# Performance work log

Hardware: AMD Instinct MI355X
Metric: run time of the kernel (lower is better)

## Reference

```python
import jax, jax.numpy as jnp
import numpy as np

N_LEVELS = 16
N_FEAT = 2
LOG2_T = 19
TABLE_SIZE = 1 << LOG2_T
COARSE = 16.0
FINE = 512.0
BOX_MIN = jnp.array([-1.0, -1.0, -1.0], jnp.float32)
BOX_MAX = jnp.array([1.0, 1.0, 1.0], jnp.float32)
# corner offsets, bit order (x, y, z) matching utils.BOX_OFFSETS / the trilinear code
OFFSETS = jnp.array([[0, 0, 0], [0, 0, 1], [0, 1, 0], [0, 1, 1],
                     [1, 0, 0], [1, 0, 1], [1, 1, 0], [1, 1, 1]], jnp.int32)
PRIMES = jnp.array([1, 2654435761, 805459861], dtype=jnp.uint32)
_b = np.exp((np.log(FINE) - np.log(COARSE)) / (N_LEVELS - 1))
RESOLUTIONS = jnp.asarray(np.floor(COARSE * _b ** np.arange(N_LEVELS)).astype(np.float32))


def setup_inputs() -> dict:
    key = jax.random.key(0)
    k1, k2 = jax.random.split(key)
    x = jax.random.uniform(k1, (1_000_000, 3), jnp.float32)  # inside the [-1,1]^3 box
    embeddings = jax.random.uniform(k2, (N_LEVELS, TABLE_SIZE, N_FEAT), jnp.float32,
                                    minval=-1e-4, maxval=1e-4)
    return {"x": x, "embeddings": embeddings}


def _hash(corners):
    # corners: (N, 8, 3) int32 -> (N, 8) int32 indices in [0, TABLE_SIZE)
    u = corners.astype(jnp.uint32) * PRIMES  # wraps mod 2^32, matching int32 wrap semantics
    h = u[..., 0] ^ u[..., 1] ^ u[..., 2]
    return (h & jnp.uint32(TABLE_SIZE - 1)).astype(jnp.int32)


def _level(x, table, res):
    grid = (BOX_MAX - BOX_MIN) / res                      # (3,)
    bl = jnp.floor((x - BOX_MIN) / grid).astype(jnp.int32)  # bottom-left voxel index (N,3)
    vmin = bl.astype(jnp.float32) * grid + BOX_MIN
    w = (x - vmin) / grid                                  # trilinear weights (N,3)
    idx = _hash(bl[:, None, :] + OFFSETS[None])            # (N,8)
    emb = table[idx]                                       # (N,8,F) gather
    # per-corner weight = prod over dims of (w if bit else 1-w) — same math as nested lerps
    cw = jnp.prod(jnp.where(OFFSETS[None].astype(bool), w[:, None, :], 1.0 - w[:, None, :]), axis=-1)
    return jnp.einsum('nk,nkf->nf', cw, emb)               # (N,F)


def reference(x, embeddings):
    x = jnp.clip(x, BOX_MIN, BOX_MAX)

    def body(_, lv):
        table, res = lv
        return None, _level(x, table, res)

    _, ys = jax.lax.scan(body, None, (embeddings, RESOLUTIONS))  # (L,N,F)
    return jnp.transpose(ys, (1, 0, 2)).reshape(x.shape[0], N_LEVELS * N_FEAT)
```

## Files before the change

kernel.cpp:

```cpp
#include <hip/hip_runtime.h>
#include <hip/hip_fp16.h>
#include <math.h>

#define N_LEVELS 16
#define LOG2_T 19
#define TABLE_SIZE (1 << LOG2_T)
#define IDX_MASK ((unsigned)(TABLE_SIZE - 1))
#define N_STAGED 4
#define N_FINE (N_LEVELS - N_STAGED)
#define DENSE_CAP 11936
#define THREADS 256
#define PTS_PER_THREAD 4
#define PTS_PER_BLOCK (THREADS * PTS_PER_THREAD)

typedef float f2_t __attribute__((ext_vector_type(2)));
typedef float f4_t __attribute__((ext_vector_type(4)));

struct Params {
    float res[N_LEVELS];
    int   c0[N_STAGED];
    int   K[N_STAGED];
    int   K2[N_STAGED];
    int   base[N_STAGED + 1];
    int   n_pts;
};

__global__ __launch_bounds__(256) void convert_fine(
    const f2_t* __restrict__ emb, unsigned* __restrict__ tab, int n)
{
    int i = blockIdx.x * 256 + threadIdx.x;
    if (i >= n) return;
    f2_t e = __builtin_nontemporal_load(&emb[(size_t)N_STAGED * TABLE_SIZE + i]);
    union { __half2 h2; unsigned u; } c;
    c.h2 = __floats2half2_rn(e.x, e.y);
    __builtin_nontemporal_store(c.u, &tab[i]);
}

__global__ __launch_bounds__(256) void build_dense(
    const f2_t* __restrict__ emb, unsigned* __restrict__ dense, Params P)
{
    int t = blockIdx.x * 256 + threadIdx.x;
    if (t >= P.base[N_STAGED]) return;
    int lev = 0;
    if (t >= P.base[1]) lev = 1;
    if (t >= P.base[2]) lev = 2;
    if (t >= P.base[3]) lev = 3;
    int li = t - P.base[lev];
    int K  = P.K[lev];
    int kx = li % K; int r2 = li / K; int ky = r2 % K; int kz = r2 / K;
    unsigned cx = (unsigned)(P.c0[lev] + kx);
    unsigned cy = (unsigned)(P.c0[lev] + ky);
    unsigned cz = (unsigned)(P.c0[lev] + kz);
    unsigned h = (cx ^ (cy * 2654435761u) ^ (cz * 805459861u)) & IDX_MASK;
    f2_t e = emb[(size_t)lev * TABLE_SIZE + h];
    union { __half2 h2; unsigned u; } c;
    c.h2 = __floats2half2_rn(e.x, e.y);
    dense[t] = c.u;
}

__device__ __forceinline__ void acc_corner(
    unsigned w0, unsigned w1, float g0, float g1, float& a0, float& a1)
{
    union { unsigned u; __half2 h; } p0, p1;
    p0.u = w0; p1.u = w1;
    a0 += g0 * __low2float(p0.h)  + g1 * __low2float(p1.h);
    a1 += g0 * __high2float(p0.h) + g1 * __high2float(p1.h);
}

__device__ __forceinline__ void level_eval(
    int lev, const Params& P, const unsigned* s_dense,
    const unsigned* __restrict__ tabF, const f2_t* __restrict__ emb,
    float xx, float xy, float xz, float& acc0, float& acc1)
{
    float r = P.res[lev];
    float grid = 2.0f / r;
    float tx = (xx + 1.0f) / grid;
    float ty = (xy + 1.0f) / grid;
    float tz = (xz + 1.0f) / grid;
    int blx = (int)floorf(tx);
    int bly = (int)floorf(ty);
    int blz = (int)floorf(tz);
    float wx = (xx - ((float)blx * grid + -1.0f)) / grid;
    float wy = (xy - ((float)bly * grid + -1.0f)) / grid;
    float wz = (xz - ((float)blz * grid + -1.0f)) / grid;

    float fy[2] = {1.0f - wy, wy};
    float fz[2] = {1.0f - wz, wz};
    float fx0 = 1.0f - wx, fx1 = wx;

    acc0 = 0.0f; acc1 = 0.0f;

    if (lev < N_STAGED) {
        int K = P.K[lev], K2 = P.K2[lev], c0 = P.c0[lev];
        int kx = blx - c0, ky = bly - c0, kz = blz - c0;
        unsigned lim = (unsigned)(K - 1);
        if ((unsigned)kx < lim && (unsigned)ky < lim && (unsigned)kz < lim) {
            int i00 = P.base[lev] + (kz * K + ky) * K + kx;
#pragma unroll
            for (int yz = 0; yz < 4; ++yz) {
                int id = i00 + (yz >> 1) * K + (yz & 1) * K2;
                float wyz = fy[yz >> 1] * fz[yz & 1];
                acc_corner(s_dense[id], s_dense[id + 1], fx0 * wyz, fx1 * wyz,
                           acc0, acc1);
            }
        } else {
            const f2_t* tab = emb + (size_t)lev * TABLE_SIZE;
#pragma unroll
            for (int k = 0; k < 8; ++k) {
                int bx = (k >> 2) & 1, by = (k >> 1) & 1, bz = k & 1;
                unsigned cx = (unsigned)(blx + bx);
                unsigned cy = (unsigned)(bly + by);
                unsigned cz = (unsigned)(blz + bz);
                unsigned h = (cx ^ (cy * 2654435761u) ^ (cz * 805459861u)) & IDX_MASK;
                f2_t e = tab[h];
                float w = (bx ? wx : 1.0f - wx) * fy[by] * fz[bz];
                acc0 += w * e.x;
                acc1 += w * e.y;
            }
        }
    } else {
        const unsigned* tab = tabF + (size_t)(lev - N_STAGED) * TABLE_SIZE;
        unsigned ux  = (unsigned)blx;
        unsigned hy0 = (unsigned)bly * 2654435761u;
        unsigned hy1 = ((unsigned)bly + 1u) * 2654435761u;
        unsigned hz0 = (unsigned)blz * 805459861u;
        unsigned hz1 = ((unsigned)blz + 1u) * 805459861u;
        unsigned w0a[4], w1a[4], i1a[4];
#pragma unroll
        for (int yz = 0; yz < 4; ++yz) {
            unsigned hyz = ((yz & 2) ? hy1 : hy0) ^ ((yz & 1) ? hz1 : hz0);
            unsigned i0 = (ux ^ hyz) & IDX_MASK;
            unsigned i1 = ((ux + 1u) ^ hyz) & IDX_MASK;
            i1a[yz] = i1;
            uint4 g = *(const uint4*)(tab + (i0 & ~3u));
            unsigned s0 = i0 & 3u, s1 = i1 & 3u;
            unsigned t0 = (s0 & 1u) ? g.y : g.x;
            unsigned t1 = (s0 & 1u) ? g.w : g.z;
            w0a[yz] = (s0 & 2u) ? t1 : t0;
            unsigned u0 = (s1 & 1u) ? g.y : g.x;
            unsigned u1 = (s1 & 1u) ? g.w : g.z;
            w1a[yz] = (s1 & 2u) ? u1 : u0;
        }
        if ((ux & 3u) == 3u) {
#pragma unroll
            for (int yz = 0; yz < 4; ++yz) w1a[yz] = tab[i1a[yz]];
        }
#pragma unroll
        for (int yz = 0; yz < 4; ++yz) {
            float wyz = fy[yz >> 1] * fz[yz & 1];
            acc_corner(w0a[yz], w1a[yz], fx0 * wyz, fx1 * wyz, acc0, acc1);
        }
    }
}

__global__ __launch_bounds__(256) void ingp_hash_fused(
    const float* __restrict__ x,
    const unsigned* __restrict__ tabF,
    const unsigned* __restrict__ denseG,
    const f2_t* __restrict__ emb,
    float* __restrict__ out,
    Params P)
{
    __shared__ __align__(16) unsigned s_dense[DENSE_CAP];
    {
        const uint4* src = (const uint4*)denseG;
        uint4* dst = (uint4*)s_dense;
#pragma unroll
        for (int i = 0; i < DENSE_CAP / 4 / THREADS + 1; ++i) {
            int id = i * THREADS + (int)threadIdx.x;
            if (id < DENSE_CAP / 4) dst[id] = src[id];
        }
    }
    __syncthreads();

    int base_pt = blockIdx.x * PTS_PER_BLOCK;
#pragma unroll 1
    for (int j = 0; j < PTS_PER_THREAD; ++j) {
        int n = base_pt + j * THREADS + (int)threadIdx.x;
        if (n >= P.n_pts) break;

        float xx = fminf(fmaxf(__builtin_nontemporal_load(&x[n * 3 + 0]), -1.0f), 1.0f);
        float xy = fminf(fmaxf(__builtin_nontemporal_load(&x[n * 3 + 1]), -1.0f), 1.0f);
        float xz = fminf(fmaxf(__builtin_nontemporal_load(&x[n * 3 + 2]), -1.0f), 1.0f);

        float* orow = out + (size_t)n * (N_LEVELS * 2);
#pragma unroll
        for (int lp = 0; lp < N_LEVELS / 2; ++lp) {
            float a0, a1, b0, b1;
            level_eval(2 * lp + 0, P, s_dense, tabF, emb, xx, xy, xz, a0, a1);
            level_eval(2 * lp + 1, P, s_dense, tabF, emb, xx, xy, xz, b0, b1);
            f4_t o4 = {a0, a1, b0, b1};
            __builtin_nontemporal_store(o4, (f4_t*)(orow + lp * 4));
        }
    }
}

__global__ __launch_bounds__(256) void ingp_hash_pair_f32(
    const float* __restrict__ x, const f2_t* __restrict__ emb,
    float* __restrict__ out, Params P)
{
    int b = blockIdx.x;
    int slot = b & 7;
    int n = (b >> 3) * 256 + (int)threadIdx.x;
    if (n >= P.n_pts) return;
    float xx = fminf(fmaxf(x[n * 3 + 0], -1.0f), 1.0f);
    float xy = fminf(fmaxf(x[n * 3 + 1], -1.0f), 1.0f);
    float xz = fminf(fmaxf(x[n * 3 + 2], -1.0f), 1.0f);
    f4_t o4;
#pragma unroll
    for (int hl = 0; hl < 2; ++hl) {
        int lev = 2 * slot + hl;
        float grid = 2.0f / P.res[lev];
        int blx = (int)floorf((xx + 1.0f) / grid);
        int bly = (int)floorf((xy + 1.0f) / grid);
        int blz = (int)floorf((xz + 1.0f) / grid);
        float wx = (xx - ((float)blx * grid + -1.0f)) / grid;
        float wy = (xy - ((float)bly * grid + -1.0f)) / grid;
        float wz = (xz - ((float)blz * grid + -1.0f)) / grid;
        const f2_t* tab = emb + (size_t)lev * TABLE_SIZE;
        float acc0 = 0.0f, acc1 = 0.0f;
#pragma unroll
        for (int k = 0; k < 8; ++k) {
            int bx = (k >> 2) & 1, by = (k >> 1) & 1, bz = k & 1;
            unsigned h = ((unsigned)(blx + bx)
                          ^ ((unsigned)(bly + by) * 2654435761u)
                          ^ ((unsigned)(blz + bz) * 805459861u)) & IDX_MASK;
            f2_t e = tab[h];
            float w = (bx ? wx : 1.0f - wx) * (by ? wy : 1.0f - wy) * (bz ? wz : 1.0f - wz);
            acc0 += w * e.x; acc1 += w * e.y;
        }
        if (hl == 0) { o4.x = acc0; o4.y = acc1; } else { o4.z = acc0; o4.w = acc1; }
    }
    __builtin_nontemporal_store(o4, (f4_t*)(out + (size_t)n * (N_LEVELS * 2) + slot * 4));
}

extern "C" void kernel_launch(void* const* d_in, const int* in_sizes, int n_in,
                              void* d_out, int out_size, void* d_ws, size_t ws_size,
                              hipStream_t stream) {
    const float* x   = (const float*)d_in[0];
    const float* emb = (const float*)d_in[1];
    float* out = (float*)d_out;
    int n_pts = in_sizes[0] / 3;

    Params P;
    double b = exp((log(512.0) - log(16.0)) / 15.0);
    for (int i = 0; i < N_LEVELS; ++i)
        P.res[i] = (float)floor(16.0 * pow(b, (double)i));
    P.n_pts = n_pts;

    int base = 0;
    for (int l = 0; l < N_STAGED; ++l) {
        float grid = 2.0f / P.res[l];
        int blmin = (int)floorf(1.0f / grid);
        int blmax = (int)floorf(2.0f / grid);
        int K = blmax - blmin + 2;
        P.c0[l] = blmin; P.K[l] = K; P.K2[l] = K * K;
        P.base[l] = base; base += K * K * K;
    }
    P.base[N_STAGED] = base;

    size_t need = (size_t)N_FINE * TABLE_SIZE * 4 + (size_t)DENSE_CAP * 4;
    if (base <= DENSE_CAP && ws_size >= need && d_ws != nullptr) {
        unsigned* tabF   = (unsigned*)d_ws;
        unsigned* denseG = tabF + (size_t)N_FINE * TABLE_SIZE;
        int nF = N_FINE * TABLE_SIZE;
        hipLaunchKernelGGL(convert_fine, dim3((nF + 255) / 256), dim3(256), 0, stream,
                           (const f2_t*)emb, tabF, nF);
        hipLaunchKernelGGL(build_dense, dim3((base + 255) / 256), dim3(256), 0, stream,
                           (const f2_t*)emb, denseG, P);
        int blocks = (n_pts + PTS_PER_BLOCK - 1) / PTS_PER_BLOCK;
        hipLaunchKernelGGL(ingp_hash_fused, dim3(blocks), dim3(256), 0, stream,
                           x, tabF, denseG, (const f2_t*)emb, out, P);
    } else {
        int blocks = 8 * ((n_pts + 255) / 256);
        hipLaunchKernelGGL(ingp_hash_pair_f32, dim3(blocks), dim3(256), 0, stream,
                           x, (const f2_t*)emb, out, P);
    }
}
```

Baseline: 628.2 us.

## Split level pairs across threads and stage only two coarse levels in LDS

Each thread now evaluates one pair of levels for a point, with 8 threads per point and 32 points per block iteration. Only levels 0-1 stay in shared memory; levels 2-3 read a 4-aligned dense table from global memory through vector loads. The aim is more parallelism per point, coalesced row writes and a much smaller LDS footprint for higher occupancy. The cost is lane divergence between coarse and fine branches and repeated x loads across the 8 threads of each point.

```diff
diff --git a/kernel.cpp b/kernel.cpp
--- a/kernel.cpp
+++ b/kernel.cpp
@@ -9,9 +9,10 @@
 #define N_STAGED 4
 #define N_FINE (N_LEVELS - N_STAGED)
 #define DENSE_CAP 11936
+#define N_LDS 2728
 #define THREADS 256
-#define PTS_PER_THREAD 4
-#define PTS_PER_BLOCK (THREADS * PTS_PER_THREAD)
+#define ITERS 16
+#define PTS_PER_BLOCK (32 * ITERS)
 
 typedef float f2_t __attribute__((ext_vector_type(2)));
 typedef float f4_t __attribute__((ext_vector_type(4)));
@@ -41,12 +42,13 @@
 {
     int t = blockIdx.x * 256 + threadIdx.x;
     if (t >= P.base[N_STAGED]) return;
-    int lev = 0;
-    if (t >= P.base[1]) lev = 1;
-    if (t >= P.base[2]) lev = 2;
-    if (t >= P.base[3]) lev = 3;
+    int lev = 3;
+    if (t < P.base[3]) lev = 2;
+    if (t < P.base[2]) lev = 1;
+    if (t < P.base[1]) lev = 0;
     int li = t - P.base[lev];
     int K  = P.K[lev];
+    if (li >= K * K * K) return;
     int kx = li % K; int r2 = li / K; int ky = r2 % K; int kz = r2 / K;
     unsigned cx = (unsigned)(P.c0[lev] + kx);
     unsigned cy = (unsigned)(P.c0[lev] + ky);
@@ -67,93 +69,114 @@
     a1 += g0 * __high2float(p0.h) + g1 * __high2float(p1.h);
 }
 
-__device__ __forceinline__ void level_eval(
-    int lev, const Params& P, const unsigned* s_dense,
-    const unsigned* __restrict__ tabF, const f2_t* __restrict__ emb,
-    float xx, float xy, float xz, float& acc0, float& acc1)
-{
-    float r = P.res[lev];
-    float grid = 2.0f / r;
-    float tx = (xx + 1.0f) / grid;
-    float ty = (xy + 1.0f) / grid;
-    float tz = (xz + 1.0f) / grid;
-    int blx = (int)floorf(tx);
-    int bly = (int)floorf(ty);
-    int blz = (int)floorf(tz);
-    float wx = (xx - ((float)blx * grid + -1.0f)) / grid;
-    float wy = (xy - ((float)bly * grid + -1.0f)) / grid;
-    float wz = (xz - ((float)blz * grid + -1.0f)) / grid;
-
-    float fy[2] = {1.0f - wy, wy};
-    float fz[2] = {1.0f - wz, wz};
+__device__ __forceinline__ unsigned pick4(uint4 g, unsigned s)
+{
+    unsigned t0 = (s & 1u) ? g.y : g.x;
+    unsigned t1 = (s & 1u) ? g.w : g.z;
+    return (s & 2u) ? t1 : t0;
+}
+
+#define GRID_SETUP(gridv)                                                  \
+    float tx = (xx + 1.0f) / (gridv);                                      \
+    float ty = (xy + 1.0f) / (gridv);                                      \
+    float tz = (xz + 1.0f) / (gridv);                                      \
+    int blx = (int)floorf(tx);                                             \
+    int bly = (int)floorf(ty);                                             \
+    int blz = (int)floorf(tz);                                             \
+    float wx = (xx - ((float)blx * (gridv) + -1.0f)) / (gridv);            \
+    float wy = (xy - ((float)bly * (gridv) + -1.0f)) / (gridv);            \
+    float wz = (xz - ((float)blz * (gridv) + -1.0f)) / (gridv);            \
+    float fy[2] = {1.0f - wy, wy};                                         \
+    float fz[2] = {1.0f - wz, wz};                                         \
     float fx0 = 1.0f - wx, fx1 = wx;
 
-    acc0 = 0.0f; acc1 = 0.0f;
-
-    if (lev < N_STAGED) {
-        int K = P.K[lev], K2 = P.K2[lev], c0 = P.c0[lev];
-        int kx = blx - c0, ky = bly - c0, kz = blz - c0;
-        unsigned lim = (unsigned)(K - 1);
-        if ((unsigned)kx < lim && (unsigned)ky < lim && (unsigned)kz < lim) {
-            int i00 = P.base[lev] + (kz * K + ky) * K + kx;
+__device__ __forceinline__ void eval_fine(
+    float grid, const unsigned* __restrict__ tab,
+    float xx, float xy, float xz, float& a0, float& a1)
+{
+    GRID_SETUP(grid)
+    unsigned ux  = (unsigned)blx;
+    unsigned hy0 = (unsigned)bly * 2654435761u;
+    unsigned hy1 = ((unsigned)bly + 1u) * 2654435761u;
+    unsigned hz0 = (unsigned)blz * 805459861u;
+    unsigned hz1 = ((unsigned)blz + 1u) * 805459861u;
+    unsigned w0a[4], w1a[4], i1a[4];
+#pragma unroll
+    for (int yz = 0; yz < 4; ++yz) {
+        unsigned hyz = ((yz & 2) ? hy1 : hy0) ^ ((yz & 1) ? hz1 : hz0);
+        unsigned i0 = (ux ^ hyz) & IDX_MASK;
+        unsigned i1 = ((ux + 1u) ^ hyz) & IDX_MASK;
+        i1a[yz] = i1;
+        uint4 g = *(const uint4*)(tab + (i0 & ~3u));
+        w0a[yz] = pick4(g, i0 & 3u);
+        w1a[yz] = pick4(g, i1 & 3u);
+    }
+    if ((ux & 3u) == 3u) {
+#pragma unroll
+        for (int yz = 0; yz < 4; ++yz) w1a[yz] = tab[i1a[yz]];
+    }
+    a0 = 0.0f; a1 = 0.0f;
+#pragma unroll
+    for (int yz = 0; yz < 4; ++yz) {
+        float wyz = fy[yz >> 1] * fz[yz & 1];
+        acc_corner(w0a[yz], w1a[yz], fx0 * wyz, fx1 * wyz, a0, a1);
+    }
+}
+
+template <int LEV, bool FROM_LDS>
+__device__ __forceinline__ void eval_coarse(
+    const Params& P, const unsigned* s_dense, const unsigned* __restrict__ denseG,
+    const f2_t* __restrict__ emb,
+    float xx, float xy, float xz, float& a0, float& a1)
+{
+    float grid = 2.0f / P.res[LEV];
+    GRID_SETUP(grid)
+    int K = P.K[LEV], K2 = P.K2[LEV];
+    int kx = blx - P.c0[LEV], ky = bly - P.c0[LEV], kz = blz - P.c0[LEV];
+    a0 = 0.0f; a1 = 0.0f;
+    unsigned lim = (unsigned)(K - 1);
+    if ((unsigned)kx < lim && (unsigned)ky < lim && (unsigned)kz < lim) {
+        int i00 = (kz * K + ky) * K + kx;
+        if (FROM_LDS) {
+            int ib = P.base[LEV] + i00;
 #pragma unroll
             for (int yz = 0; yz < 4; ++yz) {
-                int id = i00 + (yz >> 1) * K + (yz & 1) * K2;
+                int id = ib + (yz >> 1) * K + (yz & 1) * K2;
                 float wyz = fy[yz >> 1] * fz[yz & 1];
                 acc_corner(s_dense[id], s_dense[id + 1], fx0 * wyz, fx1 * wyz,
-                           acc0, acc1);
+                           a0, a1);
             }
         } else {
-            const f2_t* tab = emb + (size_t)lev * TABLE_SIZE;
-#pragma unroll
-            for (int k = 0; k < 8; ++k) {
-                int bx = (k >> 2) & 1, by = (k >> 1) & 1, bz = k & 1;
-                unsigned cx = (unsigned)(blx + bx);
-                unsigned cy = (unsigned)(bly + by);
-                unsigned cz = (unsigned)(blz + bz);
-                unsigned h = (cx ^ (cy * 2654435761u) ^ (cz * 805459861u)) & IDX_MASK;
-                f2_t e = tab[h];
-                float w = (bx ? wx : 1.0f - wx) * fy[by] * fz[bz];
-                acc0 += w * e.x;
-                acc1 += w * e.y;
+            const unsigned* tb = denseG + P.base[LEV];
+#pragma unroll
+            for (int yz = 0; yz < 4; ++yz) {
+                unsigned id = (unsigned)(i00 + (yz >> 1) * K + (yz & 1) * K2);
+                uint4 g = *(const uint4*)(tb + (id & ~3u));
+                unsigned s0 = id & 3u;
+                unsigned w0 = pick4(g, s0);
+                unsigned w1;
+                if (s0 == 3u) w1 = tb[id + 1u];
+                else          w1 = pick4(g, s0 + 1u);
+                float wyz = fy[yz >> 1] * fz[yz & 1];
+                acc_corner(w0, w1, fx0 * wyz, fx1 * wyz, a0, a1);
             }
         }
     } else {
-        const unsigned* tab = tabF + (size_t)(lev - N_STAGED) * TABLE_SIZE;
-        unsigned ux  = (unsigned)blx;
-        unsigned hy0 = (unsigned)bly * 2654435761u;
-        unsigned hy1 = ((unsigned)bly + 1u) * 2654435761u;
-        unsigned hz0 = (unsigned)blz * 805459861u;
-        unsigned hz1 = ((unsigned)blz + 1u) * 805459861u;
-        unsigned w0a[4], w1a[4], i1a[4];
-#pragma unroll
-        for (int yz = 0; yz < 4; ++yz) {
-            unsigned hyz = ((yz & 2) ? hy1 : hy0) ^ ((yz & 1) ? hz1 : hz0);
-            unsigned i0 = (ux ^ hyz) & IDX_MASK;
-            unsigned i1 = ((ux + 1u) ^ hyz) & IDX_MASK;
-            i1a[yz] = i1;
-            uint4 g = *(const uint4*)(tab + (i0 & ~3u));
-            unsigned s0 = i0 & 3u, s1 = i1 & 3u;
-            unsigned t0 = (s0 & 1u) ? g.y : g.x;
-            unsigned t1 = (s0 & 1u) ? g.w : g.z;
-            w0a[yz] = (s0 & 2u) ? t1 : t0;
-            unsigned u0 = (s1 & 1u) ? g.y : g.x;
-            unsigned u1 = (s1 & 1u) ? g.w : g.z;
-            w1a[yz] = (s1 & 2u) ? u1 : u0;
-        }
-        if ((ux & 3u) == 3u) {
-#pragma unroll
-            for (int yz = 0; yz < 4; ++yz) w1a[yz] = tab[i1a[yz]];
-        }
-#pragma unroll
-        for (int yz = 0; yz < 4; ++yz) {
-            float wyz = fy[yz >> 1] * fz[yz & 1];
-            acc_corner(w0a[yz], w1a[yz], fx0 * wyz, fx1 * wyz, acc0, acc1);
-        }
-    }
-}
-
-__global__ __launch_bounds__(256) void ingp_hash_fused(
+        const f2_t* tab = emb + (size_t)LEV * TABLE_SIZE;
+#pragma unroll
+        for (int k = 0; k < 8; ++k) {
+            int bx = (k >> 2) & 1, by = (k >> 1) & 1, bz = k & 1;
+            unsigned h = ((unsigned)(blx + bx)
+                          ^ ((unsigned)(bly + by) * 2654435761u)
+                          ^ ((unsigned)(blz + bz) * 805459861u)) & IDX_MASK;
+            f2_t e = tab[h];
+            float w = (bx ? wx : 1.0f - wx) * fy[by] * fz[bz];
+            a0 += w * e.x; a1 += w * e.y;
+        }
+    }
+}
+
+__global__ __launch_bounds__(256) void ingp_hash_v5(
     const float* __restrict__ x,
     const unsigned* __restrict__ tabF,
     const unsigned* __restrict__ denseG,
@@ -161,36 +184,51 @@
     float* __restrict__ out,
     Params P)
 {
-    __shared__ __align__(16) unsigned s_dense[DENSE_CAP];
+    __shared__ __align__(16) unsigned s_dense[N_LDS];
+    __shared__ float s_res[N_LEVELS];
     {
         const uint4* src = (const uint4*)denseG;
         uint4* dst = (uint4*)s_dense;
-#pragma unroll
-        for (int i = 0; i < DENSE_CAP / 4 / THREADS + 1; ++i) {
-            int id = i * THREADS + (int)threadIdx.x;
-            if (id < DENSE_CAP / 4) dst[id] = src[id];
-        }
+        for (int id = threadIdx.x; id < N_LDS / 4; id += THREADS) dst[id] = src[id];
+        if (threadIdx.x < N_LEVELS) s_res[threadIdx.x] = P.res[threadIdx.x];
     }
     __syncthreads();
 
-    int base_pt = blockIdx.x * PTS_PER_BLOCK;
+    int lp  = threadIdx.x & 7;
+    int ptl = threadIdx.x >> 3;
+
+    float gridA = 2.0f / s_res[2 * lp];
+    float gridB = 2.0f / s_res[2 * lp + 1];
+    int fo = 2 * lp - 4; if (fo < 0) fo = 0;
+    const unsigned* tA = tabF + (size_t)fo * TABLE_SIZE;
+    const unsigned* tB = tabF + (size_t)(fo + 1) * TABLE_SIZE;
+
+    int base_n = blockIdx.x * PTS_PER_BLOCK + ptl;
+
 #pragma unroll 1
-    for (int j = 0; j < PTS_PER_THREAD; ++j) {
-        int n = base_pt + j * THREADS + (int)threadIdx.x;
-        if (n >= P.n_pts) break;
-
-        float xx = fminf(fmaxf(__builtin_nontemporal_load(&x[n * 3 + 0]), -1.0f), 1.0f);
-        float xy = fminf(fmaxf(__builtin_nontemporal_load(&x[n * 3 + 1]), -1.0f), 1.0f);
-        float xz = fminf(fmaxf(__builtin_nontemporal_load(&x[n * 3 + 2]), -1.0f), 1.0f);
-
-        float* orow = out + (size_t)n * (N_LEVELS * 2);
-#pragma unroll
-        for (int lp = 0; lp < N_LEVELS / 2; ++lp) {
-            float a0, a1, b0, b1;
-            level_eval(2 * lp + 0, P, s_dense, tabF, emb, xx, xy, xz, a0, a1);
-            level_eval(2 * lp + 1, P, s_dense, tabF, emb, xx, xy, xz, b0, b1);
-            f4_t o4 = {a0, a1, b0, b1};
-            __builtin_nontemporal_store(o4, (f4_t*)(orow + lp * 4));
+    for (int it = 0; it < ITERS; ++it) {
+        int n = base_n + it * 32;
+        int nc = n < P.n_pts ? n : P.n_pts - 1;
+        float xx = fminf(fmaxf(__builtin_nontemporal_load(&x[nc * 3 + 0]), -1.0f), 1.0f);
+        float xy = fminf(fmaxf(__builtin_nontemporal_load(&x[nc * 3 + 1]), -1.0f), 1.0f);
+        float xz = fminf(fmaxf(__builtin_nontemporal_load(&x[nc * 3 + 2]), -1.0f), 1.0f);
+
+        float r0, r1, r2, r3;
+        if (lp == 0) {
+            eval_coarse<0, true>(P, s_dense, denseG, emb, xx, xy, xz, r0, r1);
+            eval_coarse<1, true>(P, s_dense, denseG, emb, xx, xy, xz, r2, r3);
+        } else if (lp == 1) {
+            eval_coarse<2, false>(P, s_dense, denseG, emb, xx, xy, xz, r0, r1);
+            eval_coarse<3, false>(P, s_dense, denseG, emb, xx, xy, xz, r2, r3);
+        } else {
+            eval_fine(gridA, tA, xx, xy, xz, r0, r1);
+            eval_fine(gridB, tB, xx, xy, xz, r2, r3);
+        }
+
+        if (n < P.n_pts) {
+            f4_t o4 = {r0, r1, r2, r3};
+            __builtin_nontemporal_store(
+                o4, (f4_t*)(out + (size_t)n * (N_LEVELS * 2) + lp * 4));
         }
     }
 }
@@ -206,7 +244,7 @@
     float xx = fminf(fmaxf(x[n * 3 + 0], -1.0f), 1.0f);
     float xy = fminf(fmaxf(x[n * 3 + 1], -1.0f), 1.0f);
     float xz = fminf(fmaxf(x[n * 3 + 2], -1.0f), 1.0f);
-    f4_t o4;
+    float r0 = 0.f, r1 = 0.f, r2 = 0.f, r3 = 0.f;
 #pragma unroll
     for (int hl = 0; hl < 2; ++hl) {
         int lev = 2 * slot + hl;
@@ -229,8 +267,9 @@
             float w = (bx ? wx : 1.0f - wx) * (by ? wy : 1.0f - wy) * (bz ? wz : 1.0f - wz);
             acc0 += w * e.x; acc1 += w * e.y;
         }
-        if (hl == 0) { o4.x = acc0; o4.y = acc1; } else { o4.z = acc0; o4.w = acc1; }
-    }
+        if (hl == 0) { r0 = acc0; r1 = acc1; } else { r2 = acc0; r3 = acc1; }
+    }
+    f4_t o4 = {r0, r1, r2, r3};
     __builtin_nontemporal_store(o4, (f4_t*)(out + (size_t)n * (N_LEVELS * 2) + slot * 4));
 }
 
@@ -255,12 +294,16 @@
         int blmax = (int)floorf(2.0f / grid);
         int K = blmax - blmin + 2;
         P.c0[l] = blmin; P.K[l] = K; P.K2[l] = K * K;
-        P.base[l] = base; base += K * K * K;
+        P.base[l] = base;
+        base += K * K * K;
+        base = (base + 3) & ~3;
     }
     P.base[N_STAGED] = base;
 
     size_t need = (size_t)N_FINE * TABLE_SIZE * 4 + (size_t)DENSE_CAP * 4;
-    if (base <= DENSE_CAP && ws_size >= need && d_ws != nullptr) {
+    bool ok = (base <= DENSE_CAP) && (P.base[2] == N_LDS) &&
+              (ws_size >= need) && (d_ws != nullptr);
+    if (ok) {
         unsigned* tabF   = (unsigned*)d_ws;
         unsigned* denseG = tabF + (size_t)N_FINE * TABLE_SIZE;
         int nF = N_FINE * TABLE_SIZE;
@@ -269,7 +312,7 @@
         hipLaunchKernelGGL(build_dense, dim3((base + 255) / 256), dim3(256), 0, stream,
                            (const f2_t*)emb, denseG, P);
         int blocks = (n_pts + PTS_PER_BLOCK - 1) / PTS_PER_BLOCK;
-        hipLaunchKernelGGL(ingp_hash_fused, dim3(blocks), dim3(256), 0, stream,
+        hipLaunchKernelGGL(ingp_hash_v5, dim3(blocks), dim3(256), 0, stream,
                            x, tabF, denseG, (const f2_t*)emb, out, P);
     } else {
         int blocks = 8 * ((n_pts + 255) / 256);
```

After: 661.0 us. 1.05x slower.
